# Performance work log

Measured on AMD Instinct MI355X. Metric: run time of the kernel, lower is better.

The kernel has to match this reference:

```python
import jax, jax.numpy as jnp
import numpy as np

N_NODES = 100000
N_EDGES = 1600000
N_GRAPHS = 1000
H = 4

def _ln(x, g, b, eps=1e-5):
    m = x.mean(-1, keepdims=True)
    v = ((x - m) ** 2).mean(-1, keepdims=True)
    return (x - m) / jnp.sqrt(v + eps) * g + b

def _gat(x, src, dst, W, att_src, att_dst, bias, C):
    # PyG GATConv (self-loops already appended to src/dst): per-edge scores,
    # segment softmax over incoming edges of each dst node, scatter-add aggregation.
    N = x.shape[0]
    h = (x @ W.T).reshape(N, H, C)                      # [N,H,C]
    a_s = (h * att_src[None]).sum(-1)                   # [N,H]
    a_d = (h * att_dst[None]).sum(-1)                   # [N,H]
    e = jax.nn.leaky_relu(a_s[src] + a_d[dst], 0.2)     # [E,H]
    m = jax.ops.segment_max(e, dst, num_segments=N)
    w = jnp.exp(e - m[dst])
    denom = jax.ops.segment_sum(w, dst, num_segments=N)
    alpha = w / denom[dst]
    out = jax.ops.segment_sum(alpha[:, :, None] * h[src], dst, num_segments=N)
    return out.reshape(N, H * C) + bias

def _mha_len1(y, in_w, in_b, out_w, out_b, d):
    # seq_len==1 (x.unsqueeze(0)): softmax over a single key is identically 1,
    # so MHA(y,y,y) == out_proj(v_proj(y)). Exactly the original math.
    v = y @ in_w[2 * d:3 * d].T + in_b[2 * d:3 * d]
    return v @ out_w.T + out_b

def _forward(x, edge_index, batch, fc_feat_w, fc_feat_b,
             gat1_w, gat1_as, gat1_ad, gat1_b,
             gat2_w, gat2_as, gat2_ad, gat2_b,
             enc_in_w, enc_in_b, enc_out_w, enc_out_b,
             enc_f1_w, enc_f1_b, enc_f2_w, enc_f2_b,
             enc_ln1_g, enc_ln1_b, enc_ln2_g, enc_ln2_b,
             dec_sa_in_w, dec_sa_in_b, dec_sa_out_w, dec_sa_out_b,
             dec_ca_in_w, dec_ca_in_b, dec_ca_out_w, dec_ca_out_b,
             dec_f1_w, dec_f1_b, dec_f2_w, dec_f2_b,
             dec_ln1_g, dec_ln1_b, dec_ln2_g, dec_ln2_b, dec_ln3_g, dec_ln3_b,
             fc_w, fc_b):
    N = x.shape[0]
    d = 16 * H  # 64
    loop = jnp.arange(N, dtype=edge_index.dtype)
    src = jnp.concatenate([edge_index[0], loop])  # add_self_loops=True (PyG default)
    dst = jnp.concatenate([edge_index[1], loop])
    h = x @ fc_feat_w.T + fc_feat_b                     # feature_fc: [N,8]
    h = jax.nn.leaky_relu(_gat(h, src, dst, gat1_w, gat1_as, gat1_ad, gat1_b, 32), 0.01)
    h = jax.nn.leaky_relu(_gat(h, src, dst, gat2_w, gat2_as, gat2_ad, gat2_b, 16), 0.01)
    y = h  # [N,64]; transformer sees (L=1, B=N, E=64)
    for i in range(2):  # encoder layers
        a = _mha_len1(y, enc_in_w[i], enc_in_b[i], enc_out_w[i], enc_out_b[i], d)
        y = _ln(y + a, enc_ln1_g[i], enc_ln1_b[i])
        f = jax.nn.relu(y @ enc_f1_w[i].T + enc_f1_b[i]) @ enc_f2_w[i].T + enc_f2_b[i]
        y = _ln(y + f, enc_ln2_g[i], enc_ln2_b[i])
    for i in range(2):  # decoder layers (memory == tgt)
        a = _mha_len1(y, dec_sa_in_w[i], dec_sa_in_b[i], dec_sa_out_w[i], dec_sa_out_b[i], d)
        y = _ln(y + a, dec_ln1_g[i], dec_ln1_b[i])
        a = _mha_len1(y, dec_ca_in_w[i], dec_ca_in_b[i], dec_ca_out_w[i], dec_ca_out_b[i], d)
        y = _ln(y + a, dec_ln2_g[i], dec_ln2_b[i])
        f = jax.nn.relu(y @ dec_f1_w[i].T + dec_f1_b[i]) @ dec_f2_w[i].T + dec_f2_b[i]
        y = _ln(y + f, dec_ln3_g[i], dec_ln3_b[i])
    sums = jax.ops.segment_sum(y, batch, num_segments=N_GRAPHS)
    cnts = jax.ops.segment_sum(jnp.ones((N,), y.dtype), batch, num_segments=N_GRAPHS)
    pooled = sums / jnp.maximum(cnts, 1.0)[:, None]     # global_mean_pool
    return pooled @ fc_w.T + fc_b

def setup_inputs() -> dict:
    key = jax.random.key(0)
    ks = iter(jax.random.split(key, 64))
    p = lambda *s: jax.random.normal(next(ks), s, dtype=jnp.float32) * 0.1
    d = 64
    inp = {
        'x': jax.random.normal(next(ks), (N_NODES, 4), dtype=jnp.float32),
        'edge_index': jax.random.randint(next(ks), (2, N_EDGES), 0, N_NODES, dtype=jnp.int32),
        'batch': jnp.sort(jax.random.randint(next(ks), (N_NODES,), 0, N_GRAPHS, dtype=jnp.int32)),
        'fc_feat_w': p(8, 4), 'fc_feat_b': p(8),
        'gat1_w': p(128, 8), 'gat1_as': p(H, 32), 'gat1_ad': p(H, 32), 'gat1_b': p(128),
        'gat2_w': p(64, 128), 'gat2_as': p(H, 16), 'gat2_ad': p(H, 16), 'gat2_b': p(64),
        'enc_in_w': p(2, 3 * d, d), 'enc_in_b': p(2, 3 * d), 'enc_out_w': p(2, d, d), 'enc_out_b': p(2, d),
        'enc_f1_w': p(2, 256, d), 'enc_f1_b': p(2, 256), 'enc_f2_w': p(2, d, 256), 'enc_f2_b': p(2, d),
        'enc_ln1_g': jnp.ones((2, d)), 'enc_ln1_b': jnp.zeros((2, d)),
        'enc_ln2_g': jnp.ones((2, d)), 'enc_ln2_b': jnp.zeros((2, d)),
        'dec_sa_in_w': p(2, 3 * d, d), 'dec_sa_in_b': p(2, 3 * d), 'dec_sa_out_w': p(2, d, d), 'dec_sa_out_b': p(2, d),
        'dec_ca_in_w': p(2, 3 * d, d), 'dec_ca_in_b': p(2, 3 * d), 'dec_ca_out_w': p(2, d, d), 'dec_ca_out_b': p(2, d),
        'dec_f1_w': p(2, 256, d), 'dec_f1_b': p(2, 256), 'dec_f2_w': p(2, d, 256), 'dec_f2_b': p(2, d),
        'dec_ln1_g': jnp.ones((2, d)), 'dec_ln1_b': jnp.zeros((2, d)),
        'dec_ln2_g': jnp.ones((2, d)), 'dec_ln2_b': jnp.zeros((2, d)),
        'dec_ln3_g': jnp.ones((2, d)), 'dec_ln3_b': jnp.zeros((2, d)),
        'fc_w': p(33, d), 'fc_b': p(33),
    }
    return inp

def reference(x, edge_index, batch, fc_feat_w, fc_feat_b,
              gat1_w, gat1_as, gat1_ad, gat1_b,
              gat2_w, gat2_as, gat2_ad, gat2_b,
              enc_in_w, enc_in_b, enc_out_w, enc_out_b,
              enc_f1_w, enc_f1_b, enc_f2_w, enc_f2_b,
              enc_ln1_g, enc_ln1_b, enc_ln2_g, enc_ln2_b,
              dec_sa_in_w, dec_sa_in_b, dec_sa_out_w, dec_sa_out_b,
              dec_ca_in_w, dec_ca_in_b, dec_ca_out_w, dec_ca_out_b,
              dec_f1_w, dec_f1_b, dec_f2_w, dec_f2_b,
              dec_ln1_g, dec_ln1_b, dec_ln2_g, dec_ln2_b, dec_ln3_g, dec_ln3_b,
              fc_w, fc_b):
    return _forward(x, edge_index, batch, fc_feat_w, fc_feat_b,
                    gat1_w, gat1_as, gat1_ad, gat1_b,
                    gat2_w, gat2_as, gat2_ad, gat2_b,
                    enc_in_w, enc_in_b, enc_out_w, enc_out_b,
                    enc_f1_w, enc_f1_b, enc_f2_w, enc_f2_b,
                    enc_ln1_g, enc_ln1_b, enc_ln2_g, enc_ln2_b,
                    dec_sa_in_w, dec_sa_in_b, dec_sa_out_w, dec_sa_out_b,
                    dec_ca_in_w, dec_ca_in_b, dec_ca_out_w, dec_ca_out_b,
                    dec_f1_w, dec_f1_b, dec_f2_w, dec_f2_b,
                    dec_ln1_g, dec_ln1_b, dec_ln2_g, dec_ln2_b, dec_ln3_g, dec_ln3_b,
                    fc_w, fc_b)
```

## Files before the change

### kernel.cpp

```cpp
#include <hip/hip_runtime.h>

#define NN 100000
#define NE 1600000
#define NG 1000
#define ETOT (NE + NN)
#define NODES_PER_GRP 12500

typedef _Float16 f16x8 __attribute__((ext_vector_type(8)));
typedef _Float16 f16x4 __attribute__((ext_vector_type(4)));
typedef _Float16 f16x2 __attribute__((ext_vector_type(2)));
typedef float f32x16 __attribute__((ext_vector_type(16)));
#define XROW 72

__global__ void k_h1(const float* __restrict__ x, const float* __restrict__ ffw,
                     const float* __restrict__ ffb, const float* __restrict__ g1w,
                     const float* __restrict__ asw, const float* __restrict__ adw,
                     _Float16* __restrict__ h1p, float* __restrict__ asp,
                     float* __restrict__ ad_, int* __restrict__ deg) {
    int tid = blockIdx.x * 256 + threadIdx.x;
    if (tid < NN) deg[tid] = 0;
    int n = __builtin_amdgcn_readfirstlane(tid >> 6);
    int jp = threadIdx.x & 63;
    float xv[4];
#pragma unroll
    for (int k = 0; k < 4; k++) xv[k] = x[n * 4 + k];
    float h0[8];
#pragma unroll
    for (int o = 0; o < 8; o++) {
        float a = ffb[o];
#pragma unroll
        for (int k = 0; k < 4; k++) a = fmaf(xv[k], ffw[o * 4 + k], a);
        h0[o] = a;
    }
    const float* w0 = g1w + jp * 8;
    const float* w1 = g1w + (jp + 64) * 8;
    float a0 = 0.f, a1 = 0.f;
#pragma unroll
    for (int k = 0; k < 8; k++) { a0 = fmaf(h0[k], w0[k], a0); a1 = fmaf(h0[k], w1[k], a1); }
    f16x2 r; r[0] = (_Float16)a0; r[1] = (_Float16)a1;
    *(f16x2*)(h1p + ((size_t)n * 64 + jp) * 2) = r;
    float p0 = a0 * asw[jp], p1 = a1 * asw[jp + 64];
    float d0 = a0 * adw[jp], d1 = a1 * adw[jp + 64];
#pragma unroll
    for (int m = 1; m <= 16; m <<= 1) {
        p0 += __shfl_xor(p0, m, 64); p1 += __shfl_xor(p1, m, 64);
        d0 += __shfl_xor(d0, m, 64); d1 += __shfl_xor(d1, m, 64);
    }
    if ((jp & 31) == 0) {
        int half = jp >> 5;
        *(float2*)(asp + n * 4 + half * 2) = make_float2(p0, p1);
        ad_[n * 4 + half] = d0;
        ad_[n * 4 + 2 + half] = d1;
    }
}

#define CLD(q) int ee##q = e + q * stride; \
               int d##q = (ee##q < NE) ? __builtin_nontemporal_load(ei + NE + ee##q) : -1;
#define CAT(q) if (d##q >= lo && d##q < hi) atomicAdd(&deg[d##q], 1);
__global__ void k_count(const int* __restrict__ ei, int* __restrict__ deg) {
    int g = blockIdx.x & 7;
    int bi = blockIdx.x >> 3;
    int nb = gridDim.x >> 3;
    int lo = g * NODES_PER_GRP, hi = lo + NODES_PER_GRP;
    int stride = nb * 256;
    for (int e = bi * 256 + threadIdx.x; e < NE; e += 8 * stride) {
        CLD(0) CLD(1) CLD(2) CLD(3) CLD(4) CLD(5) CLD(6) CLD(7)
        CAT(0) CAT(1) CAT(2) CAT(3) CAT(4) CAT(5) CAT(6) CAT(7)
    }
}

__global__ void k_scan1(const int* __restrict__ deg, int* __restrict__ offs, int* __restrict__ bsum) {
    __shared__ int s[1024];
    int tid = threadIdx.x;
    int i = blockIdx.x * 1024 + tid;
    int v = (i < NN) ? deg[i] + 1 : 0;
    s[tid] = v;
    __syncthreads();
    for (int d = 1; d < 1024; d <<= 1) {
        int t = 0;
        if (tid >= d) t = s[tid - d];
        __syncthreads();
        if (tid >= d) s[tid] += t;
        __syncthreads();
    }
    if (i < NN) offs[i] = s[tid] - v;
    if (tid == 1023) bsum[blockIdx.x] = s[tid];
}

__global__ void k_scan2(int* __restrict__ bsum) {
    __shared__ int s[128];
    int tid = threadIdx.x;
    int v = (tid < 98) ? bsum[tid] : 0;
    s[tid] = v;
    __syncthreads();
    for (int d = 1; d < 128; d <<= 1) {
        int t = 0;
        if (tid >= d) t = s[tid - d];
        __syncthreads();
        if (tid >= d) s[tid] += t;
        __syncthreads();
    }
    bsum[tid] = s[tid] - v;
}

__global__ void k_scan3(int* __restrict__ offs, const int* __restrict__ bsum, int* __restrict__ cur,
                        int* __restrict__ srcs) {
    int i = blockIdx.x * 1024 + threadIdx.x;
    if (i < NN) {
        int v = offs[i] + bsum[blockIdx.x];
        offs[i] = v;
        cur[i] = v + 1;
        srcs[v] = i;
    }
    if (i == 0) offs[NN] = ETOT;
}

#define SLD(q) int ee##q = e + q * stride; int d##q = -1, s##q = 0; \
               if (ee##q < NE) { d##q = __builtin_nontemporal_load(ei + NE + ee##q); \
                                 s##q = __builtin_nontemporal_load(ei + ee##q); }
#define SAT(q) if (d##q >= lo && d##q < hi) { int p = atomicAdd(&cur[d##q], 1); srcs[p] = s##q; }
__global__ void k_scatter(const int* __restrict__ ei, int* __restrict__ cur,
                          int* __restrict__ srcs) {
    int g = blockIdx.x & 7;
    int bi = blockIdx.x >> 3;
    int nb = gridDim.x >> 3;
    int lo = g * NODES_PER_GRP, hi = lo + NODES_PER_GRP;
    int stride = nb * 256;
    for (int e = bi * 256 + threadIdx.x; e < NE; e += 8 * stride) {
        SLD(0) SLD(1) SLD(2) SLD(3) SLD(4) SLD(5) SLD(6) SLD(7)
        SAT(0) SAT(1) SAT(2) SAT(3) SAT(4) SAT(5) SAT(6) SAT(7)
    }
}

__global__ void k_ew1(const int* __restrict__ offs, const int* __restrict__ srcs,
                      const float* __restrict__ asp, const float* __restrict__ ad_,
                      uint2* __restrict__ ew) {
    int t = blockIdx.x * 256 + threadIdx.x;
    int d = t >> 4, li = t & 15;
    if (d >= NN) return;
    int off = offs[d], deg = offs[d + 1] - off;
    float4 b = *(const float4*)(ad_ + d * 4);
    for (int j = li; j < deg; j += 16) {
        int s = srcs[off + j];
        float4 a = *(const float4*)(asp + s * 4);
        float e0 = a.x + b.x; e0 = fmaxf(e0, 0.2f * e0);
        float e2 = a.y + b.z; e2 = fmaxf(e2, 0.2f * e2);
        float e1 = a.z + b.y; e1 = fmaxf(e1, 0.2f * e1);
        float e3 = a.w + b.w; e3 = fmaxf(e3, 0.2f * e3);
        union { unsigned u; _Float16 h[2]; } c0, c1;
        c0.h[0] = (_Float16)__expf(e0); c0.h[1] = (_Float16)__expf(e2);
        c1.h[0] = (_Float16)__expf(e1); c1.h[1] = (_Float16)__expf(e3);
        uint2 o; o.x = c0.u; o.y = c1.u;
        ew[off + j] = o;
    }
}

__global__ void k_ew2(const int* __restrict__ offs, const int* __restrict__ srcs,
                      const float* __restrict__ as_, const float* __restrict__ ad_,
                      uint2* __restrict__ ew) {
    int t = blockIdx.x * 256 + threadIdx.x;
    int d = t >> 4, li = t & 15;
    if (d >= NN) return;
    int off = offs[d], deg = offs[d + 1] - off;
    float4 b = *(const float4*)(ad_ + d * 4);
    for (int j = li; j < deg; j += 16) {
        int s = srcs[off + j];
        float4 a = *(const float4*)(as_ + s * 4);
        float e0 = a.x + b.x; e0 = fmaxf(e0, 0.2f * e0);
        float e1 = a.y + b.y; e1 = fmaxf(e1, 0.2f * e1);
        float e2 = a.z + b.z; e2 = fmaxf(e2, 0.2f * e2);
        float e3 = a.w + b.w; e3 = fmaxf(e3, 0.2f * e3);
        union { unsigned u; _Float16 h[2]; } c0, c1;
        c0.h[0] = (_Float16)__expf(e0); c0.h[1] = (_Float16)__expf(e1);
        c1.h[0] = (_Float16)__expf(e2); c1.h[1] = (_Float16)__expf(e3);
        uint2 o; o.x = c0.u; o.y = c1.u;
        ew[off + j] = o;
    }
}

#define G1LD(q)  int s##q = sp[j + q]; uint2 e##q = wp[j + q];
#define G1LDM(q) int jj##q = j + q; int jc##q = jj##q < deg ? jj##q : deg - 1; \
                 int s##q = sp[jc##q]; uint2 e##q = wp[jc##q]; \
                 if (jj##q >= deg) { e##q.x = 0u; e##q.y = 0u; }
#define G1GA(q)  f16x2 p##q = *(const f16x2*)(h1p + (size_t)s##q * 128 + lane * 2);
#define G1AC(q, W0, W1, A0, A1) { \
    union { unsigned u; _Float16 h[2]; } c; c.u = hA ? e##q.y : e##q.x; \
    float w0 = (float)c.h[0], w1 = (float)c.h[1]; \
    W0 += w0; W1 += w1; \
    A0 = fmaf(w0, (float)p##q[0], A0); A1 = fmaf(w1, (float)p##q[1], A1); }

__global__ void k_gat1(const int* __restrict__ offs, const int* __restrict__ srcs,
                       const uint2* __restrict__ ew, const _Float16* __restrict__ h1p,
                       const float* __restrict__ bias, _Float16* __restrict__ g1h) {
    int wid = __builtin_amdgcn_readfirstlane((blockIdx.x * 256 + threadIdx.x) >> 6);
    int lane = threadIdx.x & 63;
    if (wid >= NN) return;
    int off = offs[wid];
    int deg = offs[wid + 1] - off;
    int hA = lane >> 5;
    const int* sp = srcs + off;
    const uint2* wp = ew + off;
    float ws0 = 0.f, ws1 = 0.f, ac0 = 0.f, ac1 = 0.f;
    float ws0b = 0.f, ws1b = 0.f, ac0b = 0.f, ac1b = 0.f;
    int j = 0;
    for (; j + 8 <= deg; j += 8) {
        G1LD(0) G1LD(1) G1LD(2) G1LD(3) G1LD(4) G1LD(5) G1LD(6) G1LD(7)
        G1GA(0) G1GA(1) G1GA(2) G1GA(3) G1GA(4) G1GA(5) G1GA(6) G1GA(7)
        G1AC(0, ws0, ws1, ac0, ac1)     G1AC(1, ws0b, ws1b, ac0b, ac1b)
        G1AC(2, ws0, ws1, ac0, ac1)     G1AC(3, ws0b, ws1b, ac0b, ac1b)
        G1AC(4, ws0, ws1, ac0, ac1)     G1AC(5, ws0b, ws1b, ac0b, ac1b)
        G1AC(6, ws0, ws1, ac0, ac1)     G1AC(7, ws0b, ws1b, ac0b, ac1b)
    }
    if (j < deg) {
        G1LDM(0) G1LDM(1) G1LDM(2) G1LDM(3) G1LDM(4) G1LDM(5) G1LDM(6) G1LDM(7)
        G1GA(0) G1GA(1) G1GA(2) G1GA(3) G1GA(4) G1GA(5) G1GA(6) G1GA(7)
        G1AC(0, ws0, ws1, ac0, ac1)     G1AC(1, ws0b, ws1b, ac0b, ac1b)
        G1AC(2, ws0, ws1, ac0, ac1)     G1AC(3, ws0b, ws1b, ac0b, ac1b)
        G1AC(4, ws0, ws1, ac0, ac1)     G1AC(5, ws0b, ws1b, ac0b, ac1b)
        G1AC(6, ws0, ws1, ac0, ac1)     G1AC(7, ws0b, ws1b, ac0b, ac1b)
    }
    ws0 += ws0b; ws1 += ws1b; ac0 += ac0b; ac1 += ac1b;
    float v0 = ac0 / ws0 + bias[lane];      v0 = fmaxf(v0, 0.01f * v0);
    float v1 = ac1 / ws1 + bias[lane + 64]; v1 = fmaxf(v1, 0.01f * v1);
    g1h[(size_t)wid * 128 + lane] = (_Float16)v0;
    g1h[(size_t)wid * 128 + lane + 64] = (_Float16)v1;
}

#define G2LD(q)  int s##q = sp[j + q]; uint2 e##q = wp[j + q];
#define G2LDM(q) int jj##q = j + q; int jc##q = jj##q < deg ? jj##q : deg - 1; \
                 int s##q = sp[jc##q]; uint2 e##q = wp[jc##q]; \
                 if (jj##q >= deg) { e##q.x = 0u; e##q.y = 0u; }
#define G2GA(q)  float hv##q = (float)h2h[(size_t)s##q * 64 + lane];
#define G2AC(q, W, A) { \
    unsigned sel = (hd & 2) ? e##q.y : e##q.x; \
    union { unsigned u; _Float16 h[2]; } c; c.u = sel >> sh; \
    float w = (float)c.h[0]; W += w; A = fmaf(w, hv##q, A); }

__global__ void k_gat2(const int* __restrict__ offs, const int* __restrict__ srcs,
                       const uint2* __restrict__ ew, const _Float16* __restrict__ h2h,
                       const float* __restrict__ bias, _Float16* __restrict__ g2h) {
    int wid = __builtin_amdgcn_readfirstlane((blockIdx.x * 256 + threadIdx.x) >> 6);
    int lane = threadIdx.x & 63;
    if (wid >= NN) return;
    int off = offs[wid];
    int deg = offs[wid + 1] - off;
    int hd = lane >> 4;
    int sh = (hd & 1) * 16;
    const int* sp = srcs + off;
    const uint2* wp = ew + off;
    float ws = 0.f, ac = 0.f, wsb = 0.f, acb = 0.f;
    int j = 0;
    for (; j + 8 <= deg; j += 8) {
        G2LD(0) G2LD(1) G2LD(2) G2LD(3) G2LD(4) G2LD(5) G2LD(6) G2LD(7)
        G2GA(0) G2GA(1) G2GA(2) G2GA(3) G2GA(4) G2GA(5) G2GA(6) G2GA(7)
        G2AC(0, ws, ac)  G2AC(1, wsb, acb)
        G2AC(2, ws, ac)  G2AC(3, wsb, acb)
        G2AC(4, ws, ac)  G2AC(5, wsb, acb)
        G2AC(6, ws, ac)  G2AC(7, wsb, acb)
    }
    if (j < deg) {
        G2LDM(0) G2LDM(1) G2LDM(2) G2LDM(3) G2LDM(4) G2LDM(5) G2LDM(6) G2LDM(7)
        G2GA(0) G2GA(1) G2GA(2) G2GA(3) G2GA(4) G2GA(5) G2GA(6) G2GA(7)
        G2AC(0, ws, ac)  G2AC(1, wsb, acb)
        G2AC(2, ws, ac)  G2AC(3, wsb, acb)
        G2AC(4, ws, ac)  G2AC(5, wsb, acb)
        G2AC(6, ws, ac)  G2AC(7, wsb, acb)
    }
    ws += wsb; ac += acb;
    float v = ac / ws + bias[lane]; v = fmaxf(v, 0.01f * v);
    g2h[(size_t)wid * 64 + lane] = (_Float16)v;
}

#define GROW 136
#define CROW 72
__global__ __launch_bounds__(256, 2) void k_h2m(const _Float16* __restrict__ g1h,
                                                const _Float16* __restrict__ apw2,
                                                const float* __restrict__ asw,
                                                const float* __restrict__ adw,
                                                _Float16* __restrict__ h2h,
                                                float* __restrict__ as_,
                                                float* __restrict__ ad_) {
    __shared__ _Float16 ls[4 * 32 * GROW];
    const int t = threadIdx.x;
    const int w = t >> 6, l = t & 63;
    const int col = l & 31, hf = l >> 5;
    const int wv = blockIdx.x * 4 + w;
    const int nb = wv * 32;
    if (nb >= NN) return;
    _Float16* g16 = ls + w * (32 * GROW);
    const int r = l >> 1, hb = l & 1;
    {
        int nr = nb + r; if (nr >= NN) nr = NN - 1;
        const _Float16* src = g1h + (size_t)nr * 128 + hb * 64;
        _Float16* dst = g16 + r * GROW + hb * 64;
#pragma unroll
        for (int q = 0; q < 8; q++)
            *(f16x8*)(dst + q * 8) = *(const f16x8*)(src + q * 8);
    }
    f16x8 bf[8];
#pragma unroll
    for (int ks = 0; ks < 8; ks++)
        bf[ks] = *(const f16x8*)(g16 + col * GROW + ks * 16 + hf * 8);
    f32x16 acc0, acc1;
#pragma unroll
    for (int i = 0; i < 16; i++) { acc0[i] = 0.f; acc1[i] = 0.f; }
#pragma unroll
    for (int ks = 0; ks < 8; ks++) {
        f16x8 a0 = *(const f16x8*)(apw2 + ((0 * 8 + ks) * 64 + l) * 8);
        f16x8 a1 = *(const f16x8*)(apw2 + ((1 * 8 + ks) * 64 + l) * 8);
        acc0 = __builtin_amdgcn_mfma_f32_32x32x16_f16(a0, bf[ks], acc0, 0, 0, 0);
        acc1 = __builtin_amdgcn_mfma_f32_32x32x16_f16(a1, bf[ks], acc1, 0, 0, 0);
    }
    {
        float pa0 = 0.f, pa1 = 0.f, pa2 = 0.f, pa3 = 0.f;
        float pd0 = 0.f, pd1 = 0.f, pd2 = 0.f, pd3 = 0.f;
#pragma unroll
        for (int rg = 0; rg < 4; rg++)
#pragma unroll
            for (int i = 0; i < 4; i++) {
                int rr = rg * 4 + i;
                int f = i + rg * 8 + hf * 4;
                float h0v = (float)(_Float16)acc0[rr];
                float h1v = (float)(_Float16)acc1[rr];
                float s0 = asw[f], d0v = adw[f];
                float s1 = asw[32 + f], d1v = adw[32 + f];
                if (rg < 2) { pa0 = fmaf(h0v, s0, pa0); pd0 = fmaf(h0v, d0v, pd0);
                              pa2 = fmaf(h1v, s1, pa2); pd2 = fmaf(h1v, d1v, pd2); }
                else        { pa1 = fmaf(h0v, s0, pa1); pd1 = fmaf(h0v, d0v, pd1);
                              pa3 = fmaf(h1v, s1, pa3); pd3 = fmaf(h1v, d1v, pd3); }
            }
        pa0 += __shfl_xor(pa0, 32, 64); pa1 += __shfl_xor(pa1, 32, 64);
        pa2 += __shfl_xor(pa2, 32, 64); pa3 += __shfl_xor(pa3, 32, 64);
        pd0 += __shfl_xor(pd0, 32, 64); pd1 += __shfl_xor(pd1, 32, 64);
        pd2 += __shfl_xor(pd2, 32, 64); pd3 += __shfl_xor(pd3, 32, 64);
        if (hf == 0 && nb + col < NN) {
            *(float4*)(as_ + (size_t)(nb + col) * 4) = make_float4(pa0, pa1, pa2, pa3);
            *(float4*)(ad_ + (size_t)(nb + col) * 4) = make_float4(pd0, pd1, pd2, pd3);
        }
    }
    _Float16* c16 = g16;
#pragma unroll
    for (int rg = 0; rg < 4; rg++) {
        f16x4 h0, h1;
#pragma unroll
        for (int i = 0; i < 4; i++) { h0[i] = (_Float16)acc0[rg * 4 + i]; h1[i] = (_Float16)acc1[rg * 4 + i]; }
        *(f16x4*)(c16 + col * CROW + rg * 8 + hf * 4) = h0;
        *(f16x4*)(c16 + col * CROW + 32 + rg * 8 + hf * 4) = h1;
    }
    if (nb + r < NN) {
        _Float16* dst = h2h + (size_t)(nb + r) * 64 + hb * 32;
        const _Float16* srow = c16 + r * CROW + hb * 32;
#pragma unroll
        for (int q = 0; q < 4; q++)
            *(f16x8*)(dst + q * 8) = *(const f16x8*)(srow + q * 8);
    }
}

#define APK_F1 24576
#define APK_F2 90112
#define APK_TOT 155648
__global__ void k_prep(const float* __restrict__ enc_in_w, const float* __restrict__ enc_in_b,
                       const float* __restrict__ enc_out_w, const float* __restrict__ enc_out_b,
                       const float* __restrict__ sa_in_w, const float* __restrict__ sa_in_b,
                       const float* __restrict__ sa_out_w, const float* __restrict__ sa_out_b,
                       const float* __restrict__ ca_in_w, const float* __restrict__ ca_in_b,
                       const float* __restrict__ ca_out_w, const float* __restrict__ ca_out_b,
                       const float* __restrict__ ef1, const float* __restrict__ df1,
                       const float* __restrict__ ef2, const float* __restrict__ df2,
                       const float* __restrict__ g2w,
                       _Float16* __restrict__ apk, float* __restrict__ fb,
                       _Float16* __restrict__ apw2) {
    int gt = blockIdx.x * 256 + threadIdx.x;
    if (gt < 24576) {
        int tid = gt;
        int p = tid >> 12, rr = tid & 4095, j = rr >> 6, k = rr & 63;
        int li = p & 1;
        const float *iw, *ib, *ow, *ob;
        if (p < 2)      { iw = enc_in_w + li * 12288; ib = enc_in_b + li * 192; ow = enc_out_w + li * 4096; ob = enc_out_b + li * 64; }
        else if (p < 4) { iw = sa_in_w + li * 12288;  ib = sa_in_b + li * 192;  ow = sa_out_w + li * 4096;  ob = sa_out_b + li * 64; }
        else            { iw = ca_in_w + li * 12288;  ib = ca_in_b + li * 192;  ow = ca_out_w + li * 4096;  ob = ca_out_b + li * 64; }
        float a = 0.f;
        for (int m = 0; m < 64; m++) a = fmaf(ow[j * 64 + m], iw[(128 + m) * 64 + k], a);
        int l = ((k >> 3) & 1) * 32 + (j & 31);
        apk[p * 4096 + (((j >> 5) * 4 + (k >> 4)) * 64 + l) * 8 + (k & 7)] = (_Float16)a;
        if (k == 0) {
            float fa = ob[j];
            for (int m = 0; m < 64; m++) fa = fmaf(ow[j * 64 + m], ib[128 + m], fa);
            fb[p * 64 + j] = fa;
        }
    } else {
        int tid = gt - 24576;
        if (tid < 65536) {
            int pl = tid >> 14, idx = tid & 16383;
            int mt = idx >> 11, ks = (idx >> 9) & 3, l = (idx >> 3) & 63, d = idx & 7;
            int m = mt * 32 + (l & 31), k = ks * 16 + (l >> 5) * 8 + d;
            const float* f1 = (pl < 2) ? ef1 + pl * 16384 : df1 + (pl - 2) * 16384;
            apk[APK_F1 + pl * 16384 + idx] = (_Float16)f1[m * 64 + k];
        } else if (tid < 131072) {
            int rr = tid - 65536;
            int pl = rr >> 14, idx = rr & 16383;
            int mt = idx >> 13, ks = (idx >> 9) & 15, l = (idx >> 3) & 63, d = idx & 7;
            int m = mt * 32 + (l & 31), k = ks * 16 + (l >> 5) * 8 + d;
            const float* f2 = (pl < 2) ? ef2 + pl * 16384 : df2 + (pl - 2) * 16384;
            apk[APK_F2 + pl * 16384 + idx] = (_Float16)f2[m * 256 + k];
        } else {
            int rr = tid - 131072;
            int mtks = rr >> 9, l = (rr >> 3) & 63, d = rr & 7;
            int mt = mtks >> 3, ks = mtks & 7;
            int m = mt * 32 + (l & 31), k = ks * 16 + (l >> 5) * 8 + d;
            apw2[rr] = (_Float16)g2w[m * 128 + k];
        }
    }
}

struct XQ {
    const _Float16* apk; const float* fb;
    const float* ef1b; const float* ef2b; const float* df1b; const float* df2b;
    const float* el1g; const float* el1b; const float* el2g; const float* el2b;
    const float* dl1g; const float* dl1b; const float* dl2g; const float* dl2b;
    const float* dl3g; const float* dl3b;
};

__device__ __forceinline__ void xstore(_Float16* xw, const float y[4][16], int col, int hf) {
#pragma unroll
    for (int nt = 0; nt < 2; nt++)
#pragma unroll
        for (int mt = 0; mt < 2; mt++)
#pragma unroll
            for (int rg = 0; rg < 4; rg++) {
                f16x4 h4;
#pragma unroll
                for (int i = 0; i < 4; i++) h4[i] = (_Float16)y[mt * 2 + nt][rg * 4 + i];
                *(f16x4*)(xw + (nt * 32 + col) * XROW + mt * 32 + rg * 8 + hf * 4) = h4;
            }
}

__device__ __forceinline__ void loadbf(const _Float16* xw, f16x8 bf[2][4], int col, int hf) {
#pragma unroll
    for (int nt = 0; nt < 2; nt++)
#pragma unroll
        for (int ks = 0; ks < 4; ks++)
            bf[nt][ks] = *(const f16x8*)(xw + (nt * 32 + col) * XROW + ks * 16 + hf * 8);
}

__device__ __forceinline__ void lnw(float y[4][16], const float* g, const float* b, int hf) {
#pragma unroll
    for (int nt = 0; nt < 2; nt++) {
        float s = 0.f, q = 0.f;
#pragma unroll
        for (int mt = 0; mt < 2; mt++)
#pragma unroll
            for (int r = 0; r < 16; r++) { float v = y[mt * 2 + nt][r]; s += v; q = fmaf(v, v, q); }
        s += __shfl_xor(s, 32, 64);
        q += __shfl_xor(q, 32, 64);
        float m = s * 0.015625f;
        float var = fmaf(q, 0.015625f, -m * m);
        float rs = rsqrtf(var + 1e-5f);
#pragma unroll
        for (int mt = 0; mt < 2; mt++)
#pragma unroll
            for (int rg = 0; rg < 4; rg++) {
                float4 g4 = *(const float4*)(g + mt * 32 + rg * 8 + hf * 4);
                float4 b4 = *(const float4*)(b + mt * 32 + rg * 8 + hf * 4);
                float* yp = &y[mt * 2 + nt][rg * 4];
                yp[0] = fmaf((yp[0] - m) * rs, g4.x, b4.x);
                yp[1] = fmaf((yp[1] - m) * rs, g4.y, b4.y);
                yp[2] = fmaf((yp[2] - m) * rs, g4.z, b4.z);
                yp[3] = fmaf((yp[3] - m) * rs, g4.w, b4.w);
            }
    }
}

__global__ __launch_bounds__(256, 2) void k_xform(const _Float16* __restrict__ yin,
                                                  float* __restrict__ yout, XQ P) {
    __shared__ _Float16 xs[4 * 64 * XROW];
    __shared__ _Float16 wb[8192];
    const int t = threadIdx.x;
    const int w = t >> 6, l = t & 63;
    const int col = l & 31, hf = l >> 5;
    _Float16* xw = xs + w * (64 * XROW);
    const int nb = blockIdx.x * 256 + w * 64;
    const int nn0 = nb + col, nn1 = nb + 32 + col;
    const int nc0 = nn0 < NN ? nn0 : NN - 1;
    const int nc1 = nn1 < NN ? nn1 : NN - 1;

    float y[4][16];
#pragma unroll
    for (int mt = 0; mt < 2; mt++)
#pragma unroll
        for (int nt = 0; nt < 2; nt++) {
            const _Float16* src = yin + (size_t)(nt ? nc1 : nc0) * 64 + mt * 32 + hf * 4;
#pragma unroll
            for (int rg = 0; rg < 4; rg++) {
                f16x4 v = *(const f16x4*)(src + rg * 8);
#pragma unroll
                for (int i = 0; i < 4; i++) y[mt * 2 + nt][rg * 4 + i] = (float)v[i];
            }
        }
    f16x8 bf[2][4];
    xstore(xw, y, col, hf);
    loadbf(xw, bf, col, hf);

    f16x8 r0, r1, r2, r3;
    {
        const _Float16* apA = P.apk;
        r0 = *(const f16x8*)(apA + t * 8);
        r1 = *(const f16x8*)(apA + (t + 256) * 8);
    }

#pragma unroll 1
    for (int layer = 0; layer < 4; layer++) {
        const bool enc = layer < 2;
        const int li = enc ? layer : layer - 2;
        const int nat = enc ? 1 : 2;
        const int pl = enc ? layer : 2 + li;
        const _Float16* apF1 = P.apk + APK_F1 + pl * 16384;
        const _Float16* apF2 = P.apk + APK_F2 + pl * 16384;
#pragma unroll 1
        for (int at = 0; at < nat; at++) {
            const int p = enc ? layer : (at == 0 ? 2 + li : 4 + li);
            __syncthreads();
            *(f16x8*)(wb + t * 8) = r0;
            *(f16x8*)(wb + (t + 256) * 8) = r1;
            __syncthreads();
            if (at < nat - 1) {
                const _Float16* apN = P.apk + (4 + li) * 4096;
                r0 = *(const f16x8*)(apN + t * 8);
                r1 = *(const f16x8*)(apN + (t + 256) * 8);
            } else {
                r0 = *(const f16x8*)(apF1 + t * 8);
                r1 = *(const f16x8*)(apF1 + (t + 256) * 8);
                r2 = *(const f16x8*)(apF2 + t * 8);
                r3 = *(const f16x8*)(apF2 + 8192 + t * 8);
            }
            const float* fbp = P.fb + p * 64;
            f32x16 acc[4];
#pragma unroll
            for (int mt = 0; mt < 2; mt++) {
                f32x16 a;
#pragma unroll
                for (int rg = 0; rg < 4; rg++) {
                    float4 b4 = *(const float4*)(fbp + mt * 32 + rg * 8 + hf * 4);
                    a[rg * 4 + 0] = b4.x; a[rg * 4 + 1] = b4.y; a[rg * 4 + 2] = b4.z; a[rg * 4 + 3] = b4.w;
                }
                acc[mt * 2 + 0] = a; acc[mt * 2 + 1] = a;
            }
#pragma unroll
            for (int mt = 0; mt < 2; mt++)
#pragma unroll
                for (int ks = 0; ks < 4; ks++) {
                    f16x8 af = *(const f16x8*)(wb + ((mt * 4 + ks) * 64 + l) * 8);
                    acc[mt * 2 + 0] = __builtin_amdgcn_mfma_f32_32x32x16_f16(af, bf[0][ks], acc[mt * 2 + 0], 0, 0, 0);
                    acc[mt * 2 + 1] = __builtin_amdgcn_mfma_f32_32x32x16_f16(af, bf[1][ks], acc[mt * 2 + 1], 0, 0, 0);
                }
#pragma unroll
            for (int ti = 0; ti < 4; ti++)
#pragma unroll
                for (int r = 0; r < 16; r++) y[ti][r] += acc[ti][r];
            const float *g, *b;
            if (enc)          { g = P.el1g + li * 64; b = P.el1b + li * 64; }
            else if (at == 0) { g = P.dl1g + li * 64; b = P.dl1b + li * 64; }
            else              { g = P.dl2g + li * 64; b = P.dl2b + li * 64; }
            lnw(y, g, b, hf);
            xstore(xw, y, col, hf);
            loadbf(xw, bf, col, hf);
        }
        const float* f1bp = (enc ? P.ef1b : P.df1b) + li * 256;
        const float* f2bp = (enc ? P.ef2b : P.df2b) + li * 64;
        f32x16 out[4];
#pragma unroll
        for (int mt = 0; mt < 2; mt++) {
            f32x16 a;
#pragma unroll
            for (int rg = 0; rg < 4; rg++) {
                float4 b4 = *(const float4*)(f2bp + mt * 32 + rg * 8 + hf * 4);
                a[rg * 4 + 0] = b4.x; a[rg * 4 + 1] = b4.y; a[rg * 4 + 2] = b4.z; a[rg * 4 + 3] = b4.w;
            }
            out[mt * 2 + 0] = a; out[mt * 2 + 1] = a;
        }
#pragma unroll 1
        for (int c = 0; c < 4; c++) {
            __syncthreads();
            *(f16x8*)(wb + t * 8) = r0;
            *(f16x8*)(wb + (t + 256) * 8) = r1;
            *(f16x8*)(wb + 4096 + t * 8) = r2;
            *(f16x8*)(wb + 6144 + t * 8) = r3;
            __syncthreads();
            if (c < 3) {
                r0 = *(const f16x8*)(apF1 + (c + 1) * 4096 + t * 8);
                r1 = *(const f16x8*)(apF1 + (c + 1) * 4096 + (t + 256) * 8);
                r2 = *(const f16x8*)(apF2 + (c + 1) * 2048 + t * 8);
                r3 = *(const f16x8*)(apF2 + 8192 + (c + 1) * 2048 + t * 8);
            } else if (layer < 3) {
                const _Float16* apN = P.apk + (layer + 1) * 4096;
                r0 = *(const f16x8*)(apN + t * 8);
                r1 = *(const f16x8*)(apN + (t + 256) * 8);
            }
            f32x16 ha[4];
#pragma unroll
            for (int hmt = 0; hmt < 2; hmt++) {
                f32x16 a;
#pragma unroll
                for (int rg = 0; rg < 4; rg++) {
                    float4 b4 = *(const float4*)(f1bp + c * 64 + hmt * 32 + rg * 8 + hf * 4);
                    a[rg * 4 + 0] = b4.x; a[rg * 4 + 1] = b4.y; a[rg * 4 + 2] = b4.z; a[rg * 4 + 3] = b4.w;
                }
                ha[hmt * 2 + 0] = a; ha[hmt * 2 + 1] = a;
            }
#pragma unroll
            for (int hmt = 0; hmt < 2; hmt++)
#pragma unroll
                for (int ks = 0; ks < 4; ks++) {
                    f16x8 af = *(const f16x8*)(wb + ((hmt * 4 + ks) * 64 + l) * 8);
                    ha[hmt * 2 + 0] = __builtin_amdgcn_mfma_f32_32x32x16_f16(af, bf[0][ks], ha[hmt * 2 + 0], 0, 0, 0);
                    ha[hmt * 2 + 1] = __builtin_amdgcn_mfma_f32_32x32x16_f16(af, bf[1][ks], ha[hmt * 2 + 1], 0, 0, 0);
                }
#pragma unroll
            for (int nt = 0; nt < 2; nt++)
#pragma unroll
                for (int hmt = 0; hmt < 2; hmt++)
#pragma unroll
                    for (int rg = 0; rg < 4; rg++) {
                        f16x4 h4;
#pragma unroll
                        for (int i = 0; i < 4; i++)
                            h4[i] = (_Float16)fmaxf(ha[hmt * 2 + nt][rg * 4 + i], 0.f);
                        *(f16x4*)(xw + (nt * 32 + col) * XROW + hmt * 32 + rg * 8 + hf * 4) = h4;
                    }
#pragma unroll
            for (int ksl = 0; ksl < 4; ksl++) {
                f16x8 hbf0 = *(const f16x8*)(xw + col * XROW + ksl * 16 + hf * 8);
                f16x8 hbf1 = *(const f16x8*)(xw + (32 + col) * XROW + ksl * 16 + hf * 8);
#pragma unroll
                for (int mt = 0; mt < 2; mt++) {
                    f16x8 af = *(const f16x8*)(wb + 4096 + mt * 2048 + (ksl * 64 + l) * 8);
                    out[mt * 2 + 0] = __builtin_amdgcn_mfma_f32_32x32x16_f16(af, hbf0, out[mt * 2 + 0], 0, 0, 0);
                    out[mt * 2 + 1] = __builtin_amdgcn_mfma_f32_32x32x16_f16(af, hbf1, out[mt * 2 + 1], 0, 0, 0);
                }
            }
        }
#pragma unroll
        for (int ti = 0; ti < 4; ti++)
#pragma unroll
            for (int r = 0; r < 16; r++) y[ti][r] += out[ti][r];
        const float* g2 = (enc ? P.el2g : P.dl3g) + li * 64;
        const float* b2 = (enc ? P.el2b : P.dl3b) + li * 64;
        lnw(y, g2, b2, hf);
        if (layer < 3) {
            xstore(xw, y, col, hf);
            loadbf(xw, bf, col, hf);
        }
    }
#pragma unroll
    for (int mt = 0; mt < 2; mt++)
#pragma unroll
        for (int nt = 0; nt < 2; nt++) {
            int n = nt ? nn1 : nn0;
            if (n < NN) {
                float* dst = yout + (size_t)n * 64 + mt * 32 + hf * 4;
#pragma unroll
                for (int rg = 0; rg < 4; rg++) {
                    const float* yp = &y[mt * 2 + nt][rg * 4];
                    *(float4*)(dst + rg * 8) = make_float4(yp[0], yp[1], yp[2], yp[3]);
                }
            }
        }
}

__global__ void k_pool(const float* __restrict__ y, const int* __restrict__ batch,
                       const float* __restrict__ fcw, const float* __restrict__ fcb,
                       float* __restrict__ out) {
    int b = blockIdx.x;
    int t = threadIdx.x;
    int ch = t & 63, r = t >> 6;
    int lo = 0, hi = NN;
    while (lo < hi) { int mid = (lo + hi) >> 1; if (batch[mid] < b) lo = mid + 1; else hi = mid; }
    int st = lo;
    hi = NN;
    while (lo < hi) { int mid = (lo + hi) >> 1; if (batch[mid] < b + 1) lo = mid + 1; else hi = mid; }
    int en = lo;
    float s = 0.f;
    for (int i = st + r; i < en; i += 4) s += y[(size_t)i * 64 + ch];
    __shared__ float red[256];
    __shared__ float pl[64];
    red[t] = s;
    __syncthreads();
    if (t < 64) {
        float tot = red[t] + red[t + 64] + red[t + 128] + red[t + 192];
        int cnt = en - st; if (cnt < 1) cnt = 1;
        pl[t] = tot / (float)cnt;
    }
    __syncthreads();
    if (t < 33) {
        const float* wv = fcw + t * 64;
        float a0 = 0.f, a1 = 0.f, a2 = 0.f, a3 = 0.f;
#pragma unroll
        for (int k = 0; k < 16; k++) {
            a0 = fmaf(pl[4 * k], wv[4 * k], a0);
            a1 = fmaf(pl[4 * k + 1], wv[4 * k + 1], a1);
            a2 = fmaf(pl[4 * k + 2], wv[4 * k + 2], a2);
            a3 = fmaf(pl[4 * k + 3], wv[4 * k + 3], a3);
        }
        out[b * 33 + t] = fcb[t] + (a0 + a1) + (a2 + a3);
    }
}

extern "C" void kernel_launch(void* const* d_in, const int* in_sizes, int n_in,
                              void* d_out, int out_size, void* d_ws, size_t ws_size,
                              hipStream_t stream) {
    (void)in_sizes; (void)n_in; (void)out_size; (void)ws_size;
    char* ws = (char*)d_ws;
    size_t o = 0;
    auto A = [&](size_t b) { size_t r = o; o += (b + 255) & ~(size_t)255; return r; };
    _Float16* h1p = (_Float16*)(ws + A((size_t)NN * 128 * 2));
    _Float16* h2h = (_Float16*)(ws + A((size_t)NN * 64 * 2));
    _Float16* g1h = (_Float16*)(ws + A((size_t)NN * 128 * 2));
    _Float16* g2h = (_Float16*)(ws + A((size_t)NN * 64 * 2));
    float* f_y   = (float*)(ws + A((size_t)NN * 64 * 4));
    float* f_asp = (float*)(ws + A((size_t)NN * 4 * 4));
    float* f_ad1 = (float*)(ws + A((size_t)NN * 4 * 4));
    float* f_as2 = (float*)(ws + A((size_t)NN * 4 * 4));
    float* f_ad2 = (float*)(ws + A((size_t)NN * 4 * 4));
    int* i_off   = (int*)(ws + A((size_t)(NN + 1) * 4));
    int* i_cur   = (int*)(ws + A((size_t)NN * 4));
    int* i_deg   = (int*)(ws + A((size_t)NN * 4));
    int* i_bsum  = (int*)(ws + A((size_t)1024 * 4));
    int* i_srcs  = (int*)(ws + A((size_t)ETOT * 4));
    uint2* e_w   = (uint2*)(ws + A((size_t)ETOT * 8));
    float* f_fb  = (float*)(ws + A((size_t)6 * 64 * 4));
    _Float16* f_apk = (_Float16*)(ws + A((size_t)APK_TOT * 2));
    _Float16* apw2  = (_Float16*)(ws + A((size_t)8192 * 2));

    const float* x   = (const float*)d_in[0];
    const int* ei    = (const int*)d_in[1];
    const int* batch = (const int*)d_in[2];
    #define F32(i) ((const float*)d_in[i])

    k_h1<<<NN * 64 / 256, 256, 0, stream>>>(x, F32(3), F32(4), F32(5), F32(6), F32(7),
                                            h1p, f_asp, f_ad1, i_deg);
    k_count<<<8 * 256, 256, 0, stream>>>(ei, i_deg);
    k_scan1<<<98, 1024, 0, stream>>>(i_deg, i_off, i_bsum);
    k_scan2<<<1, 128, 0, stream>>>(i_bsum);
    k_scan3<<<98, 1024, 0, stream>>>(i_off, i_bsum, i_cur, i_srcs);
    k_scatter<<<8 * 256, 256, 0, stream>>>(ei, i_cur, i_srcs);
    k_ew1<<<NN * 16 / 256, 256, 0, stream>>>(i_off, i_srcs, f_asp, f_ad1, e_w);
    k_gat1<<<NN * 64 / 256, 256, 0, stream>>>(i_off, i_srcs, e_w, h1p, F32(8), g1h);
    k_prep<<<640, 256, 0, stream>>>(F32(13), F32(14), F32(15), F32(16),
                                    F32(25), F32(26), F32(27), F32(28),
                                    F32(29), F32(30), F32(31), F32(32),
                                    F32(17), F32(33), F32(19), F32(35), F32(9),
                                    f_apk, f_fb, apw2);
    k_h2m<<<(NN / 32 + 3) / 4, 256, 0, stream>>>(g1h, apw2, F32(10), F32(11), h2h, f_as2, f_ad2);
    k_ew2<<<NN * 16 / 256, 256, 0, stream>>>(i_off, i_srcs, f_as2, f_ad2, e_w);
    k_gat2<<<NN * 64 / 256, 256, 0, stream>>>(i_off, i_srcs, e_w, h2h, F32(12), g2h);
    XQ Q;
    Q.apk = f_apk; Q.fb = f_fb;
    Q.ef1b = F32(18); Q.ef2b = F32(20);
    Q.df1b = F32(34); Q.df2b = F32(36);
    Q.el1g = F32(21); Q.el1b = F32(22); Q.el2g = F32(23); Q.el2b = F32(24);
    Q.dl1g = F32(37); Q.dl1b = F32(38); Q.dl2g = F32(39); Q.dl2b = F32(40);
    Q.dl3g = F32(41); Q.dl3b = F32(42);
    k_xform<<<(NN + 255) / 256, 256, 0, stream>>>(g2h, f_y, Q);
    k_pool<<<NG, 256, 0, stream>>>(f_y, batch, F32(43), F32(44), (float*)d_out);
    #undef F32
}
```

Baseline: 574.2 us.

## Use single-wave blocks in xform kernel and drop barrier-based weight prefetch

Restructures k_xform so each block is one 64-thread wave handling 64 nodes, with its own shared-memory weight buffer. Weights are copied directly from global memory into LDS before each GEMM, replacing the register double-buffering across four waves and the __syncthreads barriers. This removes cross-wave synchronisation stalls and allows more independent blocks per CU. The cost is four times the weight traffic through L2/LDS and the loss of load/compute overlap from prefetching.

```diff
diff --git a/kernel.cpp b/kernel.cpp
--- a/kernel.cpp
+++ b/kernel.cpp
@@ -471,15 +471,15 @@
     }
 }
 
-__global__ __launch_bounds__(256, 2) void k_xform(const _Float16* __restrict__ yin,
-                                                  float* __restrict__ yout, XQ P) {
-    __shared__ _Float16 xs[4 * 64 * XROW];
+__global__ __launch_bounds__(64, 4) void k_xform(const _Float16* __restrict__ yin,
+                                                 float* __restrict__ yout, XQ P) {
+    __shared__ _Float16 xs[64 * XROW];
     __shared__ _Float16 wb[8192];
     const int t = threadIdx.x;
-    const int w = t >> 6, l = t & 63;
+    const int l = t;
     const int col = l & 31, hf = l >> 5;
-    _Float16* xw = xs + w * (64 * XROW);
-    const int nb = blockIdx.x * 256 + w * 64;
+    _Float16* xw = xs;
+    const int nb = blockIdx.x * 64;
     const int nn0 = nb + col, nn1 = nb + 32 + col;
     const int nc0 = nn0 < NN ? nn0 : NN - 1;
     const int nc1 = nn1 < NN ? nn1 : NN - 1;
@@ -500,13 +500,6 @@
     f16x8 bf[2][4];
     xstore(xw, y, col, hf);
     loadbf(xw, bf, col, hf);
-
-    f16x8 r0, r1, r2, r3;
-    {
-        const _Float16* apA = P.apk;
-        r0 = *(const f16x8*)(apA + t * 8);
-        r1 = *(const f16x8*)(apA + (t + 256) * 8);
-    }
 
 #pragma unroll 1
     for (int layer = 0; layer < 4; layer++) {
@@ -519,20 +512,10 @@
 #pragma unroll 1
         for (int at = 0; at < nat; at++) {
             const int p = enc ? layer : (at == 0 ? 2 + li : 4 + li);
-            __syncthreads();
-            *(f16x8*)(wb + t * 8) = r0;
-            *(f16x8*)(wb + (t + 256) * 8) = r1;
-            __syncthreads();
-            if (at < nat - 1) {
-                const _Float16* apN = P.apk + (4 + li) * 4096;
-                r0 = *(const f16x8*)(apN + t * 8);
-                r1 = *(const f16x8*)(apN + (t + 256) * 8);
-            } else {
-                r0 = *(const f16x8*)(apF1 + t * 8);
-                r1 = *(const f16x8*)(apF1 + (t + 256) * 8);
-                r2 = *(const f16x8*)(apF2 + t * 8);
-                r3 = *(const f16x8*)(apF2 + 8192 + t * 8);
-            }
+            const _Float16* apA = P.apk + p * 4096;
+#pragma unroll
+            for (int i = 0; i < 8; i++)
+                *(f16x8*)(wb + (t + i * 64) * 8) = *(const f16x8*)(apA + (t + i * 64) * 8);
             const float* fbp = P.fb + p * 64;
             f32x16 acc[4];
 #pragma unroll
@@ -580,21 +563,13 @@
         }
 #pragma unroll 1
         for (int c = 0; c < 4; c++) {
-            __syncthreads();
-            *(f16x8*)(wb + t * 8) = r0;
-            *(f16x8*)(wb + (t + 256) * 8) = r1;
-            *(f16x8*)(wb + 4096 + t * 8) = r2;
-            *(f16x8*)(wb + 6144 + t * 8) = r3;
-            __syncthreads();
-            if (c < 3) {
-                r0 = *(const f16x8*)(apF1 + (c + 1) * 4096 + t * 8);
-                r1 = *(const f16x8*)(apF1 + (c + 1) * 4096 + (t + 256) * 8);
-                r2 = *(const f16x8*)(apF2 + (c + 1) * 2048 + t * 8);
-                r3 = *(const f16x8*)(apF2 + 8192 + (c + 1) * 2048 + t * 8);
-            } else if (layer < 3) {
-                const _Float16* apN = P.apk + (layer + 1) * 4096;
-                r0 = *(const f16x8*)(apN + t * 8);
-                r1 = *(const f16x8*)(apN + (t + 256) * 8);
+#pragma unroll
+            for (int i = 0; i < 8; i++)
+                *(f16x8*)(wb + (t + i * 64) * 8) = *(const f16x8*)(apF1 + c * 4096 + (t + i * 64) * 8);
+#pragma unroll
+            for (int i = 0; i < 4; i++) {
+                *(f16x8*)(wb + 4096 + (t + i * 64) * 8) = *(const f16x8*)(apF2 + c * 2048 + (t + i * 64) * 8);
+                *(f16x8*)(wb + 6144 + (t + i * 64) * 8) = *(const f16x8*)(apF2 + 8192 + c * 2048 + (t + i * 64) * 8);
             }
             f32x16 ha[4];
 #pragma unroll
@@ -760,7 +735,7 @@
     Q.el1g = F32(21); Q.el1b = F32(22); Q.el2g = F32(23); Q.el2b = F32(24);
     Q.dl1g = F32(37); Q.dl1b = F32(38); Q.dl2g = F32(39); Q.dl2b = F32(40);
     Q.dl3g = F32(41); Q.dl3b = F32(42);
-    k_xform<<<(NN + 255) / 256, 256, 0, stream>>>(g2h, f_y, Q);
+    k_xform<<<(NN + 63) / 64, 64, 0, stream>>>(g2h, f_y, Q);
     k_pool<<<NG, 256, 0, stream>>>(f_y, batch, F32(43), F32(44), (float*)d_out);
     #undef F32
 }
```

Measured after the change: 579.8 us. About the same (+1.0%).
